# Performance work log

Hardware: AMD Instinct MI355X
Metric: run time of the kernel (lower is better)

The kernel has to match this reference:

```python
import jax, jax.numpy as jnp
import numpy as np

_SAMPLING_EPS = 1e-5


def setup_inputs() -> dict:
    key = jax.random.key(0)
    k1, k2, k3, k4, k5 = jax.random.split(key, 5)
    B, V = 128, 128000
    logits = jax.random.normal(k1, (B, V), dtype=jnp.float32)
    temperature = jax.random.uniform(k2, (B,), dtype=jnp.float32)  # some rows < eps -> greedy
    top_k = jax.random.randint(k3, (B,), 1, 64, dtype=jnp.int32)   # in [1, 63]
    top_p = jax.random.uniform(k4, (B,), dtype=jnp.float32, minval=0.05, maxval=1.0)
    noise_u = jax.random.uniform(k5, (B, V), dtype=jnp.float32, minval=1e-10, maxval=1.0)
    return {"logits": logits, "temperature": temperature, "top_k": top_k,
            "top_p": top_p, "noise_u": noise_u, "max_num_logprobs": 5}


def _apply_top_k_top_p(logits, k, p):
    # Faithful to vLLM: ascending sort, top-k threshold mask, top-p cumsum mask, scatter back.
    B, V = logits.shape
    order = jnp.argsort(logits, axis=-1)                       # ascending, [B, V]
    logits_sort = jnp.take_along_axis(logits, order, axis=-1)
    neg_inf = jnp.float32(-jnp.inf)
    # top-k: pivot value at position V - k; everything strictly below it -> -inf
    pivot_idx = (V - k.astype(jnp.int32))[:, None]             # [B, 1]
    pivot = jnp.take_along_axis(logits_sort, pivot_idx, axis=-1)
    logits_sort = jnp.where(logits_sort < pivot, neg_inf, logits_sort)
    # top-p: softmax over sorted logits, cumsum, drop prefix with mass <= 1 - p (keep last)
    probs_sort = jax.nn.softmax(logits_sort, axis=-1)
    probs_sum = jnp.cumsum(probs_sort, axis=-1)
    top_p_mask = probs_sum <= (1.0 - p)[:, None]
    top_p_mask = top_p_mask.at[:, -1].set(False)
    logits_sort = jnp.where(top_p_mask, neg_inf, logits_sort)
    # scatter back to original vocab order
    rows = jnp.arange(B)[:, None]
    return jnp.zeros_like(logits).at[rows, order].set(logits_sort)


def reference(logits, temperature, top_k, top_p, noise_u, max_num_logprobs):
    # temperature scaling (temp < eps means greedy; divide by 1.0 instead)
    temp = jnp.where(temperature < _SAMPLING_EPS, 1.0, temperature)
    logits = logits.astype(jnp.float32) / temp[:, None]
    # top-k / top-p filtering
    logits = _apply_top_k_top_p(logits, top_k, top_p)
    # probabilities and sampling
    probs = jax.nn.softmax(logits, axis=-1)
    greedy = jnp.argmax(probs, axis=-1)
    q = -jnp.log(noise_u)                                      # Exp(1) noise (q.exponential_())
    random = jnp.argmax(probs / q, axis=-1)
    sampled = jnp.where(temperature < _SAMPLING_EPS, greedy, random).astype(jnp.int32)
    # top-k logprobs
    logprobs = jax.nn.log_softmax(logits, axis=-1)
    topk_logprobs, topk_indices = jax.lax.top_k(logprobs, max_num_logprobs)
    return sampled, topk_indices.astype(jnp.int32), topk_logprobs
```

## Files before the change

### kernel.cpp

```cpp
#include <hip/hip_runtime.h>
#include <math.h>
#include <stdint.h>

#define BT     256
#define TOPC   64
#define FT     512
#define SLOTS  32
#define NPART  8
#define CAPR   4096
#define CAPF   1024

__device__ __forceinline__ unsigned f2ord(float f) {
    unsigned u = __float_as_uint(f);
    return u ^ ((u & 0x80000000u) ? 0xFFFFFFFFu : 0x80000000u);
}
__device__ __forceinline__ float ord2f(unsigned k) {
    unsigned u = (k & 0x80000000u) ? (k ^ 0x80000000u) : (k ^ 0xFFFFFFFFu);
    return __uint_as_float(u);
}

__device__ unsigned radix_select_compact4(uint2* s_buf, uint2* s_keep,
                                          unsigned (*s_hist)[16], unsigned* p_cnt2,
                                          unsigned n, int tid, int wid)
{
    unsigned prefix = 0u;
    int remaining = TOPC;
    for (int shift = 28; shift >= 0; shift -= 4) {
        if (tid < 64) ((unsigned*)s_hist)[tid] = 0u;
        __syncthreads();
        for (unsigned i = (unsigned)tid; i < n; i += BT) {
            unsigned k = s_buf[i].x;
            bool ing = (shift == 28) || ((k >> (shift + 4)) == (prefix >> (shift + 4)));
            if (ing) atomicAdd(&s_hist[wid][(k >> shift) & 15u], 1u);
        }
        __syncthreads();
        int cum = 0; int b = 0; unsigned hb = 0u;
        for (int bb = 15; bb >= 0; --bb) {
            unsigned h = s_hist[0][bb] + s_hist[1][bb] + s_hist[2][bb] + s_hist[3][bb];
            cum += (int)h;
            if (cum >= remaining) { b = bb; hb = h; break; }
        }
        remaining -= (cum - (int)hb);
        prefix |= ((unsigned)b) << shift;
        __syncthreads();
    }
    if (tid == 0) *p_cnt2 = 0u;
    __syncthreads();
    for (unsigned i = (unsigned)tid; i < n; i += BT) {
        uint2 c = s_buf[i];
        if (c.x > prefix) s_keep[atomicAdd(p_cnt2, 1u)] = c;
    }
    __syncthreads();
    for (unsigned i = (unsigned)tid; i < n; i += BT) {
        uint2 c = s_buf[i];
        if (c.x == prefix) {
            unsigned pos = atomicAdd(p_cnt2, 1u);
            if (pos < TOPC) s_keep[pos] = c;
        }
    }
    __syncthreads();
    return prefix;
}

__global__ __launch_bounds__(64) void row_thresh(
    const float* __restrict__ logits, unsigned* __restrict__ thr,
    unsigned* __restrict__ ovf, int V)
{
    const int r    = blockIdx.x;
    const int lane = threadIdx.x;
    const float* rowp = logits + (size_t)r * (size_t)V;

    unsigned kr[64];
    #pragma unroll
    for (int g = 0; g < 8; ++g) {
        int c0 = g * 512 + lane * 8;
        if (c0 < V) {
            float4 a = *(const float4*)(rowp + c0);
            float4 b = *(const float4*)(rowp + c0 + 4);
            kr[g * 8 + 0] = f2ord(a.x); kr[g * 8 + 1] = f2ord(a.y);
            kr[g * 8 + 2] = f2ord(a.z); kr[g * 8 + 3] = f2ord(a.w);
            kr[g * 8 + 4] = f2ord(b.x); kr[g * 8 + 5] = f2ord(b.y);
            kr[g * 8 + 6] = f2ord(b.z); kr[g * 8 + 7] = f2ord(b.w);
        } else {
            #pragma unroll
            for (int j = 0; j < 8; ++j) kr[g * 8 + j] = 0u;
        }
    }

    unsigned lo = 0u, hi = 0xFFFFu;
    while (lo < hi) {
        unsigned mid = (lo + hi + 1u) >> 1;
        unsigned t = mid << 16;
        int c = 0;
        #pragma unroll
        for (int j = 0; j < 64; ++j) c += __popcll(__ballot(kr[j] >= t));
        if (c >= TOPC) lo = mid; else hi = mid - 1u;
    }
    if (lane == 0) { thr[r] = lo << 16; ovf[r] = 0u; }
}

__global__ __launch_bounds__(BT) void filter_pass(
    const float* __restrict__ logits, const unsigned* __restrict__ thr,
    unsigned* __restrict__ ovf, uint2* __restrict__ surv,
    int B, int V, int tpr, int slots)
{
    const int tid  = threadIdx.x;
    const int wid  = tid >> 6;
    const int lane = tid & 63;
    const unsigned long long ltm = (1ull << lane) - 1ull;
    const int nw = gridDim.x * (BT / 64);
    const int ntiles = B * tpr;

    for (int tw = blockIdx.x * (BT / 64) + wid; tw < ntiles; tw += nw) {
        const int t    = __builtin_amdgcn_readfirstlane(tw);
        const int row  = t / tpr;
        const int tin  = t - row * tpr;
        const int col0 = tin * FT + lane * 8;
        const bool v   = col0 < V;
        const float* rowp = logits + (size_t)row * (size_t)V;

        unsigned k[8];
        if (v) {
            float4 a = *(const float4*)(rowp + col0);
            float4 b = *(const float4*)(rowp + col0 + 4);
            k[0] = f2ord(a.x); k[1] = f2ord(a.y); k[2] = f2ord(a.z); k[3] = f2ord(a.w);
            k[4] = f2ord(b.x); k[5] = f2ord(b.y); k[6] = f2ord(b.z); k[7] = f2ord(b.w);
        } else {
            #pragma unroll
            for (int j = 0; j < 8; ++j) k[j] = 0u;
        }

        const unsigned tr = thr[row];
        uint2* base = surv + (size_t)t * (unsigned)slots;

        unsigned tot = 0u;
        #pragma unroll
        for (int j = 0; j < 8; ++j) {
            bool pa = v && (k[j] >= tr);
            unsigned long long m = __ballot(pa);
            if (pa) {
                unsigned pos = tot + (unsigned)__popcll(m & ltm);
                if (pos < (unsigned)slots)
                    base[pos] = make_uint2(k[j], (unsigned)(col0 + j));
            }
            tot += (unsigned)__popcll(m);
        }
        if (lane < slots && (unsigned)lane >= tot)
            base[lane] = make_uint2(0u, 0u);
        if (lane == 0 && tot > (unsigned)slots)
            atomicOr(&ovf[row], 1u);
    }
}

__global__ __launch_bounds__(BT) void reduce_slots(
    const uint2* __restrict__ surv, uint2* __restrict__ cand,
    int tpr, int slots, int npart)
{
    __shared__ uint2    s_buf[CAPR];
    __shared__ uint2    s_keep[TOPC];
    __shared__ unsigned s_hist[4][16];
    __shared__ unsigned s_cnt2;

    const int r    = blockIdx.y;
    const int part = blockIdx.x;
    const int tid  = threadIdx.x;
    const int wid  = tid >> 6;

    const int tslots = tpr * slots;
    const int share  = (tslots + npart - 1) / npart;
    const int start  = part * share;
    int end = start + share; if (end > tslots) end = tslots;
    int nn = end - start; if (nn < 0) nn = 0;

    const uint2* rs = surv + (size_t)r * (unsigned)tslots + start;
    for (int i = tid; i < nn; i += BT)
        s_buf[i] = rs[i];
    unsigned n = (unsigned)nn;
    if (n < TOPC) {
        for (unsigned i = n + (unsigned)tid; i < TOPC; i += BT)
            s_buf[i] = make_uint2(0u, 0u);
        n = TOPC;
    }
    __syncthreads();

    radix_select_compact4(s_buf, s_keep, s_hist, &s_cnt2, n, tid, wid);
    if (tid < TOPC)
        cand[((size_t)r * (unsigned)npart + (unsigned)part) * TOPC + tid] = s_keep[tid];
}

__global__ __launch_bounds__(BT) void phase2_final(
    const uint2* __restrict__ cand, const unsigned* __restrict__ ovf,
    const unsigned* __restrict__ thr, const float* __restrict__ logits,
    const float* __restrict__ temperature,
    const int*   __restrict__ top_k,
    const float* __restrict__ top_p,
    const float* __restrict__ noise_u,
    float* __restrict__ out,
    int B, int V, int M, int nc)
{
    __shared__ uint2    s_buf[CAPF];
    __shared__ uint2    s_keep[TOPC];
    __shared__ unsigned s_hist[4][16];
    __shared__ unsigned s_cnt, s_cnt2, s_ovf;
    __shared__ float    sval[TOPC], se[TOPC], sq[TOPC];
    __shared__ int      sidx[TOPC];

    const int r   = blockIdx.x;
    const int tid = threadIdx.x;
    const int wid = tid >> 6;

    const bool fb = (ovf[r] != 0u);
    unsigned n;

    if (!fb) {
        n = (unsigned)nc;
        for (unsigned i = (unsigned)tid; i < n; i += BT)
            s_buf[i] = cand[(size_t)r * (unsigned)nc + i];
        __syncthreads();
    } else {
        const float* rowp = logits + (size_t)r * (size_t)V;
        if (tid == 0) { s_cnt = 0u; s_ovf = 0u; }
        __syncthreads();
        unsigned vst = thr[r];
        bool strict = false;
        for (int t = 0; t < V; t += BT * 8) {
            int bs = t + tid * 8;
            bool v = bs < V;
            unsigned kk[8];
            if (v) {
                float4 a = *(const float4*)(rowp + bs);
                float4 b = *(const float4*)(rowp + bs + 4);
                kk[0] = f2ord(a.x); kk[1] = f2ord(a.y); kk[2] = f2ord(a.z); kk[3] = f2ord(a.w);
                kk[4] = f2ord(b.x); kk[5] = f2ord(b.y); kk[6] = f2ord(b.z); kk[7] = f2ord(b.w);
            } else {
                #pragma unroll
                for (int j = 0; j < 8; ++j) kk[j] = 0u;
            }
            unsigned pm = 0u; int np = 0;
            if (v) {
                #pragma unroll
                for (int j = 0; j < 8; ++j) {
                    bool pa = strict ? (kk[j] > vst) : (kk[j] >= vst);
                    if (pa) { pm |= (1u << j); ++np; }
                }
            }
            for (;;) {
                if (np) {
                    unsigned pos = atomicAdd(&s_cnt, (unsigned)np);
                    unsigned rem = 0u; int nr = 0;
                    #pragma unroll
                    for (int j = 0; j < 8; ++j) {
                        if (pm & (1u << j)) {
                            if (pos < CAPF) s_buf[pos] = make_uint2(kk[j], (unsigned)(bs + j));
                            else { rem |= (1u << j); ++nr; }
                            ++pos;
                        }
                    }
                    if (nr) s_ovf = 1u;
                    pm = rem; np = nr;
                }
                __syncthreads();
                unsigned o = s_ovf;
                __syncthreads();
                if (!o) break;
                unsigned nn2 = s_cnt; if (nn2 > CAPF) nn2 = CAPF;
                unsigned v2s = radix_select_compact4(s_buf, s_keep, s_hist, &s_cnt2,
                                                     nn2, tid, wid);
                if (tid < TOPC) s_buf[tid] = s_keep[tid];
                if (tid == 0) { s_cnt = TOPC; s_ovf = 0u; }
                __syncthreads();
                unsigned rem = 0u; int nr = 0;
                #pragma unroll
                for (int j = 0; j < 8; ++j)
                    if ((pm & (1u << j)) && kk[j] > v2s) { rem |= (1u << j); ++nr; }
                pm = rem; np = nr;
                vst = v2s; strict = true;
            }
        }
        n = s_cnt; if (n > CAPF) n = CAPF;
        if (n < TOPC) {
            for (unsigned i = n + (unsigned)tid; i < TOPC; i += BT)
                s_buf[i] = make_uint2(0u, 0u);
            n = TOPC;
            __syncthreads();
        }
    }

    radix_select_compact4(s_buf, s_keep, s_hist, &s_cnt2, n, tid, wid);

    for (int kk = 2; kk <= TOPC; kk <<= 1) {
        for (int j = kk >> 1; j > 0; j >>= 1) {
            if (tid < TOPC / 2) {
                int i0 = ((tid & ~(j - 1)) << 1) | (tid & (j - 1));
                int i1 = i0 | j;
                bool up = ((i0 & kk) == 0);
                uint2 A = s_keep[i0], Bv = s_keep[i1];
                bool gt = (A.x < Bv.x) || (A.x == Bv.x && A.y > Bv.y);
                if (gt == up) { s_keep[i0] = Bv; s_keep[i1] = A; }
            }
            __syncthreads();
        }
    }

    float temp_orig = temperature[r];
    float temp = (temp_orig < 1e-5f) ? 1.0f : temp_orig;

    if (tid < TOPC) {
        unsigned k = s_keep[tid].x;
        int id = (int)s_keep[tid].y;
        sval[tid] = ord2f(k) / temp;
        sidx[tid] = id;
        float u = noise_u[(size_t)r * (size_t)V + id];
        sq[tid] = -logf(u);
    }
    __syncthreads();
    if (tid < TOPC) se[tid] = expf(sval[tid] - sval[0]);
    __syncthreads();

    if (tid == 0) {
        int k = top_k[r];
        if (k < 1) k = 1; if (k > TOPC) k = TOPC;
        float p = top_p[r];

        float pivot = sval[k - 1];
        int m = k;
        while (m < TOPC && sval[m] >= pivot) ++m;

        float sum = 0.f;
        for (int i = 0; i < m; ++i) sum += se[i];

        float thr1 = 1.0f - p;
        float S = 0.f;
        int f = 1;
        for (int i = m - 1; i >= 1; --i) {
            S += se[i] / sum;
            if (S > thr1) { f = i + 1; break; }
        }

        float sum2 = 0.f;
        for (int i = 0; i < f; ++i) sum2 += se[i];

        int greedy = sidx[0];
        float best = -1.f; int bidx = 0x7fffffff;
        for (int i = 0; i < f; ++i) {
            float ratio = (se[i] / sum2) / sq[i];
            if (ratio > best || (ratio == best && sidx[i] < bidx)) {
                best = ratio; bidx = sidx[i];
            }
        }
        int sampled = (temp_orig < 1e-5f) ? greedy : bidx;

        float lse = logf(sum2);
        out[r] = (float)sampled;
        float* oidx = out + B + (size_t)r * M;
        float* olp  = out + B + (size_t)B * M + (size_t)r * M;
        int produced = 0;
        for (int i = 0; i < f && produced < M; ++i, ++produced) {
            oidx[produced] = (float)sidx[i];
            olp[produced]  = (sval[i] - sval[0]) - lse;
        }
        int v = 0;
        while (produced < M) {
            bool used = false;
            for (int i = 0; i < f; ++i) if (sidx[i] == v) { used = true; break; }
            if (!used) { oidx[produced] = (float)v; olp[produced] = -3.0e38f; ++produced; }
            ++v;
        }
    }
}

extern "C" void kernel_launch(void* const* d_in, const int* in_sizes, int n_in,
                              void* d_out, int out_size, void* d_ws, size_t ws_size,
                              hipStream_t stream)
{
    const float* logits      = (const float*)d_in[0];
    const float* temperature = (const float*)d_in[1];
    const int*   top_k       = (const int*)d_in[2];
    const float* top_p       = (const float*)d_in[3];
    const float* noise_u     = (const float*)d_in[4];

    const int B = in_sizes[1];
    const int V = in_sizes[0] / B;
    const int M = (out_size / B - 1) / 2;

    const int tpr = (V + FT - 1) / FT;

    unsigned* thr = (unsigned*)d_ws;
    unsigned* ovf = thr + B;
    size_t off1 = (((size_t)2 * B * sizeof(unsigned)) + 7) & ~(size_t)7;
    uint2* cand = (uint2*)((char*)d_ws + off1);
    size_t off2 = off1 + (size_t)B * NPART * TOPC * sizeof(uint2);
    uint2* surv = (uint2*)((char*)d_ws + off2);

    int slots = SLOTS;
    if (ws_size > off2) {
        size_t avail = (ws_size - off2) / ((size_t)B * tpr * sizeof(uint2));
        if (avail < (size_t)slots) slots = (int)avail;
    } else slots = 1;
    if (slots < 1) slots = 1;

    const int ntiles = B * tpr;
    int fblocks = (ntiles + 3) / 4;
    if (fblocks > 2048) fblocks = 2048;

    row_thresh<<<B, 64, 0, stream>>>(logits, thr, ovf, V);
    filter_pass<<<fblocks, BT, 0, stream>>>(logits, thr, ovf, surv,
                                            B, V, tpr, slots);
    dim3 gr(NPART, B);
    reduce_slots<<<gr, BT, 0, stream>>>(surv, cand, tpr, slots, NPART);
    phase2_final<<<B, BT, 0, stream>>>(cand, ovf, thr, logits,
                                       temperature, top_k, top_p, noise_u,
                                       (float*)d_out, B, V, M, NPART * TOPC);
}
```

Baseline: 193.5 us.

## Fold slot reduction stage into final per-row kernel with larger shared buffer

Removes the intermediate reduce_slots kernel, which split each row's survivor slots across 8 blocks to produce candidate lists. The final per-row kernel now loads all survivor slots for its row, up to 8192 entries, directly into shared memory and runs the radix select there. This saves one kernel launch and the candidate round-trip through global memory. In exchange, it gives up the 8-way per-row parallelism in the reduction and raises each block's shared-memory footprint, which can lower occupancy.

```diff
diff --git a/kernel.cpp b/kernel.cpp
--- a/kernel.cpp
+++ b/kernel.cpp
@@ -6,9 +6,7 @@
 #define TOPC   64
 #define FT     512
 #define SLOTS  32
-#define NPART  8
-#define CAPR   4096
-#define CAPF   1024
+#define CAPC   8192
 
 __device__ __forceinline__ unsigned f2ord(float f) {
     unsigned u = __float_as_uint(f);
@@ -152,53 +150,17 @@
     }
 }
 
-__global__ __launch_bounds__(BT) void reduce_slots(
-    const uint2* __restrict__ surv, uint2* __restrict__ cand,
-    int tpr, int slots, int npart)
-{
-    __shared__ uint2    s_buf[CAPR];
-    __shared__ uint2    s_keep[TOPC];
-    __shared__ unsigned s_hist[4][16];
-    __shared__ unsigned s_cnt2;
-
-    const int r    = blockIdx.y;
-    const int part = blockIdx.x;
-    const int tid  = threadIdx.x;
-    const int wid  = tid >> 6;
-
-    const int tslots = tpr * slots;
-    const int share  = (tslots + npart - 1) / npart;
-    const int start  = part * share;
-    int end = start + share; if (end > tslots) end = tslots;
-    int nn = end - start; if (nn < 0) nn = 0;
-
-    const uint2* rs = surv + (size_t)r * (unsigned)tslots + start;
-    for (int i = tid; i < nn; i += BT)
-        s_buf[i] = rs[i];
-    unsigned n = (unsigned)nn;
-    if (n < TOPC) {
-        for (unsigned i = n + (unsigned)tid; i < TOPC; i += BT)
-            s_buf[i] = make_uint2(0u, 0u);
-        n = TOPC;
-    }
-    __syncthreads();
-
-    radix_select_compact4(s_buf, s_keep, s_hist, &s_cnt2, n, tid, wid);
-    if (tid < TOPC)
-        cand[((size_t)r * (unsigned)npart + (unsigned)part) * TOPC + tid] = s_keep[tid];
-}
-
-__global__ __launch_bounds__(BT) void phase2_final(
-    const uint2* __restrict__ cand, const unsigned* __restrict__ ovf,
+__global__ __launch_bounds__(BT) void phase2_combined(
+    const uint2* __restrict__ surv, const unsigned* __restrict__ ovf,
     const unsigned* __restrict__ thr, const float* __restrict__ logits,
     const float* __restrict__ temperature,
     const int*   __restrict__ top_k,
     const float* __restrict__ top_p,
     const float* __restrict__ noise_u,
     float* __restrict__ out,
-    int B, int V, int M, int nc)
-{
-    __shared__ uint2    s_buf[CAPF];
+    int B, int V, int M, int tpr, int slots)
+{
+    __shared__ uint2    s_buf[CAPC];
     __shared__ uint2    s_keep[TOPC];
     __shared__ unsigned s_hist[4][16];
     __shared__ unsigned s_cnt, s_cnt2, s_ovf;
@@ -209,13 +171,20 @@
     const int tid = threadIdx.x;
     const int wid = tid >> 6;
 
-    const bool fb = (ovf[r] != 0u);
+    const int tslots = tpr * slots;
+    const bool fb = (ovf[r] != 0u) || (tslots > CAPC);
     unsigned n;
 
     if (!fb) {
-        n = (unsigned)nc;
-        for (unsigned i = (unsigned)tid; i < n; i += BT)
-            s_buf[i] = cand[(size_t)r * (unsigned)nc + i];
+        const uint2* rs = surv + (size_t)r * (unsigned)tslots;
+        for (int i = tid; i < tslots; i += BT)
+            s_buf[i] = rs[i];
+        n = (unsigned)tslots;
+        if (n < TOPC) {
+            for (unsigned i = n + (unsigned)tid; i < TOPC; i += BT)
+                s_buf[i] = make_uint2(0u, 0u);
+            n = TOPC;
+        }
         __syncthreads();
     } else {
         const float* rowp = logits + (size_t)r * (size_t)V;
@@ -251,7 +220,7 @@
                     #pragma unroll
                     for (int j = 0; j < 8; ++j) {
                         if (pm & (1u << j)) {
-                            if (pos < CAPF) s_buf[pos] = make_uint2(kk[j], (unsigned)(bs + j));
+                            if (pos < CAPC) s_buf[pos] = make_uint2(kk[j], (unsigned)(bs + j));
                             else { rem |= (1u << j); ++nr; }
                             ++pos;
                         }
@@ -263,7 +232,7 @@
                 unsigned o = s_ovf;
                 __syncthreads();
                 if (!o) break;
-                unsigned nn2 = s_cnt; if (nn2 > CAPF) nn2 = CAPF;
+                unsigned nn2 = s_cnt; if (nn2 > CAPC) nn2 = CAPC;
                 unsigned v2s = radix_select_compact4(s_buf, s_keep, s_hist, &s_cnt2,
                                                      nn2, tid, wid);
                 if (tid < TOPC) s_buf[tid] = s_keep[tid];
@@ -277,7 +246,7 @@
                 vst = v2s; strict = true;
             }
         }
-        n = s_cnt; if (n > CAPF) n = CAPF;
+        n = s_cnt; if (n > CAPC) n = CAPC;
         if (n < TOPC) {
             for (unsigned i = n + (unsigned)tid; i < TOPC; i += BT)
                 s_buf[i] = make_uint2(0u, 0u);
@@ -387,17 +356,16 @@
 
     unsigned* thr = (unsigned*)d_ws;
     unsigned* ovf = thr + B;
-    size_t off1 = (((size_t)2 * B * sizeof(unsigned)) + 7) & ~(size_t)7;
-    uint2* cand = (uint2*)((char*)d_ws + off1);
-    size_t off2 = off1 + (size_t)B * NPART * TOPC * sizeof(uint2);
-    uint2* surv = (uint2*)((char*)d_ws + off2);
+    size_t off = (((size_t)2 * B * sizeof(unsigned)) + 7) & ~(size_t)7;
+    uint2* surv = (uint2*)((char*)d_ws + off);
 
     int slots = SLOTS;
-    if (ws_size > off2) {
-        size_t avail = (ws_size - off2) / ((size_t)B * tpr * sizeof(uint2));
+    if (ws_size > off) {
+        size_t avail = (ws_size - off) / ((size_t)B * tpr * sizeof(uint2));
         if (avail < (size_t)slots) slots = (int)avail;
     } else slots = 1;
     if (slots < 1) slots = 1;
+    while (slots > 1 && tpr * slots > CAPC) --slots;
 
     const int ntiles = B * tpr;
     int fblocks = (ntiles + 3) / 4;
@@ -406,9 +374,7 @@
     row_thresh<<<B, 64, 0, stream>>>(logits, thr, ovf, V);
     filter_pass<<<fblocks, BT, 0, stream>>>(logits, thr, ovf, surv,
                                             B, V, tpr, slots);
-    dim3 gr(NPART, B);
-    reduce_slots<<<gr, BT, 0, stream>>>(surv, cand, tpr, slots, NPART);
-    phase2_final<<<B, BT, 0, stream>>>(cand, ovf, thr, logits,
-                                       temperature, top_k, top_p, noise_u,
-                                       (float*)d_out, B, V, M, NPART * TOPC);
-}
+    phase2_combined<<<B, BT, 0, stream>>>(surv, ovf, thr, logits,
+                                          temperature, top_k, top_p, noise_u,
+                                          (float*)d_out, B, V, M, tpr, slots);
+}
```

After: 213.4 us. 10.3% more time.
